# Kernel tuning notes

Measured on AMD Instinct MI355X. Metric: run time of the kernel, lower is better.

## Reference

```python
import jax, jax.numpy as jnp
import numpy as np

EPS = 1e-5
BLOCKS = 8

def _bn(x, g, b, m, v):
    # eval-mode BatchNorm1d over channel dim of [B, C, T]
    return g[:, None] * (x - m[:, None]) * jax.lax.rsqrt(v[:, None] + EPS) + b[:, None]

def _conv1x1(x, w):
    # x: [B, Cin, T], w: [Cout, Cin] -> [B, Cout, T]
    return jnp.einsum('bct,oc->bot', x, w)

def _dwconv(x, w, dil):
    # x: [B, C, T], w: [C, K] depthwise dilated conv, 'same' padding
    C, K = w.shape
    pad = dil * (K - 1) // 2
    return jax.lax.conv_general_dilated(
        x, w[:, None, :], window_strides=(1,), padding=[(pad, pad)],
        rhs_dilation=(dil,), dimension_numbers=('NCH', 'OIH', 'NCH'),
        feature_group_count=C)

def setup_inputs() -> dict:
    key = jax.random.key(0)
    ks = jax.random.split(key, 16)
    B, Cb, H, T, K = 16, 256, 512, 4096, 3
    d = {}
    d['x'] = jax.random.normal(ks[0], (B, Cb, T), jnp.float32)
    d['bn1_gamma'] = jax.random.uniform(ks[1], (BLOCKS, Cb), jnp.float32)
    d['bn1_beta'] = jax.random.normal(ks[2], (BLOCKS, Cb), jnp.float32)
    d['bn1_mean'] = jax.random.normal(ks[3], (BLOCKS, Cb), jnp.float32)
    d['bn1_var'] = jax.random.uniform(ks[4], (BLOCKS, Cb), jnp.float32)
    d['w1'] = jax.random.normal(ks[5], (BLOCKS, H, Cb), jnp.float32)
    d['bn2_gamma'] = jax.random.uniform(ks[6], (BLOCKS, H), jnp.float32)
    d['bn2_beta'] = jax.random.normal(ks[7], (BLOCKS, H), jnp.float32)
    d['bn2_mean'] = jax.random.normal(ks[8], (BLOCKS, H), jnp.float32)
    d['bn2_var'] = jax.random.uniform(ks[9], (BLOCKS, H), jnp.float32)
    d['dw_w'] = jax.random.normal(ks[10], (BLOCKS, H, K), jnp.float32)
    d['bn3_gamma'] = jax.random.uniform(ks[11], (BLOCKS, H), jnp.float32)
    d['bn3_beta'] = jax.random.normal(ks[12], (BLOCKS, H), jnp.float32)
    d['bn3_mean'] = jax.random.normal(ks[13], (BLOCKS, H), jnp.float32)
    d['bn3_var'] = jax.random.uniform(ks[14], (BLOCKS, H), jnp.float32)
    d['w2'] = jax.random.normal(ks[15], (BLOCKS, Cb, H), jnp.float32)
    return d

def reference(x, bn1_gamma, bn1_beta, bn1_mean, bn1_var, w1,
              bn2_gamma, bn2_beta, bn2_mean, bn2_var, dw_w,
              bn3_gamma, bn3_beta, bn3_mean, bn3_var, w2):
    sign = jnp.sign  # binary activation on inputs and weights
    resid = x
    for i in range(BLOCKS):
        dil = 2 ** i
        h = _bn(resid, bn1_gamma[i], bn1_beta[i], bn1_mean[i], bn1_var[i])
        h = _conv1x1(sign(h), sign(w1[i]))                 # 1x1, Cb -> H
        h = _bn(h, bn2_gamma[i], bn2_beta[i], bn2_mean[i], bn2_var[i])
        h = _dwconv(sign(h), sign(dw_w[i]), dil)           # depthwise dilated
        h = _bn(h, bn3_gamma[i], bn3_beta[i], bn3_mean[i], bn3_var[i])
        h = _conv1x1(sign(h), sign(w2[i]))                 # 1x1, H -> Cb
        resid = resid + h
    return resid
```

## Files before the change

kernel.cpp:

```cpp
#include <hip/hip_runtime.h>
#include <stdint.h>

namespace {
constexpr int Bn  = 16;
constexpr int Cc  = 256;
constexpr int Hn  = 512;
constexpr int Tn  = 4096;
constexpr int CWn = Cc / 32;
constexpr int HWn = Hn / 32;
constexpr int TWn = Tn / 32;
constexpr int TC  = 64;
constexpr float EPSf = 1e-5f;
}

typedef __attribute__((ext_vector_type(4)))  int i32x4;
typedef __attribute__((ext_vector_type(16))) int i32x16;

__device__ __forceinline__ uint32_t nib_expand(uint32_t w, int p) {
  return (((w >> p) & 0xFu) * 0x00204081u) & 0x01010101u;
}

__global__ __launch_bounds__(256) void setup_kernel(
    const float* __restrict__ bn1g, const float* __restrict__ bn1b,
    const float* __restrict__ bn1m, const float* __restrict__ bn1v,
    const float* __restrict__ w1,
    const float* __restrict__ bn2g, const float* __restrict__ bn2b,
    const float* __restrict__ bn2m, const float* __restrict__ bn2v,
    const float* __restrict__ dww,
    const float* __restrict__ bn3g, const float* __restrict__ bn3b,
    const float* __restrict__ bn3m, const float* __restrict__ bn3v,
    const float* __restrict__ w2,
    float* __restrict__ thr1, float* __restrict__ thr2, float* __restrict__ thr3,
    uint32_t* __restrict__ dws, uint32_t* __restrict__ W1p,
    uint8_t* __restrict__ W1f, int* __restrict__ Sw1, int* __restrict__ T2i,
    uint8_t* __restrict__ W2uf, int* __restrict__ Sw2)
{
  const int idx = blockIdx.x * 256 + threadIdx.x;
  if (idx < 8 * Hn * CWn) {
    const int w = idx & (CWn - 1);
    const int h = idx >> 3;
    const float* src = w1 + (size_t)h * Cc + w * 32;
    uint32_t word = 0;
#pragma unroll
    for (int j = 0; j < 32; ++j) word |= (uint32_t)(src[j] > 0.f) << j;
    W1p[h * CWn + w] = word;
    atomicAdd(&Sw1[h], (int)__popc(word));
    const int blk = h >> 9, hl = h & 511;
    uint32_t* dst = (uint32_t*)(W1f + (size_t)blk * 131072);
#pragma unroll
    for (int q = 0; q < 8; ++q)
      dst[((w * 2 + (q >> 2)) * 512 + hl) * 4 + (q & 3)] = nib_expand(word, 4 * q);
  } else {
    const int k = idx - 8 * Hn * CWn;
    const int w = k & (HWn - 1);
    const int c = k >> 4;
    const float* src = w2 + (size_t)c * Hn + w * 32;
    uint32_t word = 0;
#pragma unroll
    for (int j = 0; j < 32; ++j) word |= (uint32_t)(src[j] > 0.f) << j;
    atomicAdd(&Sw2[c], (int)__popc(word));
    const int blk = c >> 8, cl = c & 255;
    uint32_t* dst = (uint32_t*)(W2uf + (size_t)blk * 131072);
#pragma unroll
    for (int q = 0; q < 8; ++q)
      dst[((w * 2 + (q >> 2)) * 256 + cl) * 4 + (q & 3)] = nib_expand(word, 4 * q);
  }
  if (idx < 8 * Cc)
    thr1[idx] = bn1m[idx] - bn1b[idx] * sqrtf(bn1v[idx] + EPSf) / bn1g[idx];
  if (idx < 8 * Hn) {
    const float th2 = bn2m[idx] - bn2b[idx] * sqrtf(bn2v[idx] + EPSf) / bn2g[idx];
    thr2[idx] = th2;
    int T;
    if (th2 >= 8.0e6f)       T =  (1 << 24);
    else if (th2 <= -8.0e6f) T = -(1 << 24);
    else if (th2 == th2)     T = (int)floorf(th2) + 1;
    else                     T =  (1 << 24);
    T2i[idx] = T;
    thr3[idx] = bn3m[idx] - bn3b[idx] * sqrtf(bn3v[idx] + EPSf) / bn3g[idx];
    uint32_t dw = 0;
    for (int k2 = 0; k2 < 3; ++k2) dw |= (uint32_t)(dww[(size_t)idx * 3 + k2] > 0.f) << k2;
    dws[idx] = dw;
  }
}

__global__ __launch_bounds__(256) void k1_pack(
    const float* __restrict__ resid, const float* __restrict__ thr1,
    uint32_t* __restrict__ Xp)
{
  const int idx = blockIdx.x * 256 + threadIdx.x;
  const int t  = idx & (Tn - 1);
  const int cw = (idx >> 12) & (CWn - 1);
  const int b  = idx >> 15;
  const float* r = resid + ((size_t)(b * Cc + cw * 32)) * Tn + t;
  uint32_t word = 0;
#pragma unroll
  for (int j = 0; j < 32; ++j)
    word |= (uint32_t)(r[(size_t)j * Tn] > thr1[cw * 32 + j]) << j;
  Xp[((size_t)b * CWn + cw) * Tn + t] = word;
}

__global__ __launch_bounds__(256) void k2_gemm1(
    const uint32_t* __restrict__ Xp, const uint32_t* __restrict__ W1p,
    const float* __restrict__ thr2, uint32_t* __restrict__ Y)
{
  const int bid  = blockIdx.x;
  const int tblk = bid & 15;
  const int og   = (bid >> 4) & 63;
  const int b    = bid >> 10;
  const int t    = tblk * 256 + threadIdx.x;
  const int o    = og * 8;

  const uint32_t* xrow = Xp + (size_t)b * CWn * Tn + t;
  const uint32_t* wrow = W1p + o * CWn;
  int acc[8] = {0, 0, 0, 0, 0, 0, 0, 0};
#pragma unroll
  for (int w = 0; w < CWn; ++w) {
    const uint32_t xw = xrow[(size_t)w * Tn];
#pragma unroll
    for (int r = 0; r < 8; ++r)
      acc[r] += __popc(xw ^ wrow[r * CWn + w]);
  }
  const int lane = threadIdx.x & 63;
#pragma unroll
  for (int r = 0; r < 8; ++r) {
    const float v = (float)(Cc - 2 * acc[r]);
    const uint64_t m = __ballot(v > thr2[o + r]);
    if ((lane & 31) == 0)
      Y[((size_t)b * TWn + (t >> 5)) * Hn + o + r] = (uint32_t)(m >> lane);
  }
}

__global__ __launch_bounds__(512) void k_iter(
    const uint32_t* __restrict__ Yin, const uint32_t* __restrict__ dws,
    const float* __restrict__ thr3,
    const uint8_t* __restrict__ W2uf, const int* __restrict__ Sw2_i,
    const float* __restrict__ rin, float* __restrict__ rout,
    const float* __restrict__ thr1n,
    const uint8_t* __restrict__ W1f_n, const int* __restrict__ Sw1_n,
    const int* __restrict__ T2i_n, uint32_t* __restrict__ Yout,
    int dil, int do_next)
{
  __shared__ __align__(16) uint8_t Zi8[TC * 512];
  __shared__ uint32_t XpL[TC][9];
  __shared__ int   Tc[Hn];
  __shared__ float thr1L[Cc];
  __shared__ int   Sw2x2L[Cc];
  __shared__ int   Sx[TC], Sz[TC];

  const int chunk = blockIdx.x & (Tn / TC - 1);
  const int b     = blockIdx.x >> 6;
  const int tid   = threadIdx.x;
  const int lane  = tid & 63;
  const int wid   = __builtin_amdgcn_readfirstlane(tid >> 6);
  const int lh    = lane & 31;
  const int twL   = lane >> 5;
  const int tw0   = chunk * 2;
  const int half  = lane >> 5;

  if (tid < TC) { Sx[tid] = 0; Sz[tid] = 0; }
  if (tid < Cc) { thr1L[tid] = thr1n[tid]; Sw2x2L[tid] = 2 * Sw2_i[tid]; }
  Tc[tid] = T2i_n[tid] + 2 * Sw1_n[tid] - 256;
  __syncthreads();

  int zcnt = 0;
#pragma unroll
  for (int task = 0; task < 2; ++task) {
    const int hw = wid * 2 + task;
    const int tw = tw0 + twL;
    const int ch = hw * 32 + lh;

    const uint32_t* yb = Yin + (size_t)b * TWn * Hn + ch;
    const uint32_t ycur = yb[(size_t)tw * Hn];
    uint32_t yl, yr, Vl, Vr;
    if (dil >= 32) {
      const int dw = dil >> 5;
      const bool lok = tw >= dw, rok = tw + dw < TWn;
      yl = lok ? yb[(size_t)(tw - dw) * Hn] : 0u;
      yr = rok ? yb[(size_t)(tw + dw) * Hn] : 0u;
      Vl = lok ? ~0u : 0u;
      Vr = rok ? ~0u : 0u;
    } else {
      const uint32_t yp = (tw > 0) ? yb[(size_t)(tw - 1) * Hn] : 0u;
      const uint32_t yn = (tw < TWn - 1) ? yb[(size_t)(tw + 1) * Hn] : 0u;
      yl = (ycur << dil) | ((tw > 0) ? (yp >> (32 - dil)) : 0u);
      yr = (ycur >> dil) | ((tw < TWn - 1) ? (yn << (32 - dil)) : 0u);
      Vl = (tw == 0) ? (~0u << dil) : ~0u;
      Vr = (tw == TWn - 1) ? (~0u >> dil) : ~0u;
    }
    const uint32_t d = dws[ch];
    const uint32_t a  = ((d & 1u) ? yl : ~yl) & Vl;
    const uint32_t bb = (d & 2u) ? ycur : ~ycur;
    const uint32_t c  = ((d & 4u) ? yr : ~yr) & Vr;

    const float thr = thr3[ch];
    const float v3 = (thr + 3.f) * 0.5f;
    const float v2 = (thr + 2.f) * 0.5f;
    const int K3 = (int)(v3 >= 0.f) + (int)(v3 >= 1.f) + (int)(v3 >= 2.f) + (int)(v3 >= 3.f);
    const int K2 = (int)(v2 >= 0.f) + (int)(v2 >= 1.f) + (int)(v2 >= 2.f);

    const uint32_t g1 = a | bb | c;
    const uint32_t g2 = (a & bb) | (c & (a | bb));
    const uint32_t g3 = a & bb & c;
    const uint32_t full = (K3 == 0) ? ~0u : (K3 == 1) ? g1 : (K3 == 2) ? g2
                        : (K3 == 3) ? g3 : 0u;
    const uint32_t lm = (K2 == 0) ? ~0u : (K2 == 1) ? (bb | c) : (K2 == 2) ? (bb & c) : 0u;
    const uint32_t rm = (K2 == 0) ? ~0u : (K2 == 1) ? (a | bb) : (K2 == 2) ? (a & bb) : 0u;

    uint32_t w = (Vl & Vr & full) | (~Vl & lm) | (~Vr & rm);

#pragma unroll
    for (int s = 16; s; s >>= 1) {
      const uint32_t m = 0xFFFFFFFFu / ((1u << s) + 1u);
      const uint32_t o = __shfl_xor(w, s, 64);
      w = ((lane & s) == 0) ? ((w & m) | ((o & m) << s))
                            : ((w & ~m) | ((o & ~m) >> s));
    }
    const int swzA = (lane & 15) << 4;
    uint32_t e[8];
#pragma unroll
    for (int q = 0; q < 8; ++q)
      e[q] = nib_expand(w, 4 * q);
    i32x4 v0; v0[0] = e[0]; v0[1] = e[1]; v0[2] = e[2]; v0[3] = e[3];
    i32x4 v1; v1[0] = e[4]; v1[1] = e[5]; v1[2] = e[6]; v1[3] = e[7];
    *(i32x4*)&Zi8[lane * 512 + ((hw * 32)      ^ swzA)] = v0;
    *(i32x4*)&Zi8[lane * 512 + ((hw * 32 + 16) ^ swzA)] = v1;
    zcnt += (int)__popc(w);
  }
  atomicAdd(&Sz[lane], zcnt);
  __syncthreads();

  {
    const int mc   = wid;
    const int lrow = mc * 32 + lh;
    const int t0   = chunk * TC;

    float rv0[16], rv1[16];
#pragma unroll
    for (int r = 0; r < 16; ++r) {
      const int cr = mc * 32 + (r & 3) + 8 * (r >> 2) + 4 * half;
      const float* rowp = rin + ((size_t)(b * Cc + cr)) * Tn + t0;
      rv0[r] = rowp[lh];
      rv1[r] = rowp[32 + lh];
    }

    const int swz0 = (lh & 15) << 4;
    i32x16 acc0 = {0,0,0,0, 0,0,0,0, 0,0,0,0, 0,0,0,0};
    i32x16 acc1 = {0,0,0,0, 0,0,0,0, 0,0,0,0, 0,0,0,0};
#pragma unroll
    for (int kg = 0; kg < 2; ++kg) {
      i32x4 afv[8];
#pragma unroll
      for (int kk = 0; kk < 8; ++kk) {
        const int ks = kg * 8 + kk;
        afv[kk] = *(const i32x4*)(W2uf + (((size_t)(ks * 2 + half) * 256 + lrow) * 16));
      }
#pragma unroll
      for (int kk = 0; kk < 8; ++kk) {
        const int ks = kg * 8 + kk;
        const int k0 = ks * 32 + half * 16;
        const i32x4 bf0 = *(const i32x4*)&Zi8[lh * 512 + (k0 ^ swz0)];
        const i32x4 bf1 = *(const i32x4*)&Zi8[(32 + lh) * 512 + (k0 ^ swz0)];
        acc0 = __builtin_amdgcn_mfma_i32_32x32x32_i8(afv[kk], bf0, acc0, 0, 0, 0);
        acc1 = __builtin_amdgcn_mfma_i32_32x32x32_i8(afv[kk], bf1, acc1, 0, 0, 0);
      }
    }

    const int Sz0 = 2 * Sz[lh], Sz1 = 2 * Sz[32 + lh];
    uint32_t xw0 = 0, xw1 = 0;
#pragma unroll
    for (int r = 0; r < 16; ++r) {
      const int cloc = (r & 3) + 8 * (r >> 2) + 4 * half;
      const int cr = mc * 32 + cloc;
      const int sw2 = Sw2x2L[cr];
      const float th = thr1L[cr];
      float* orow = rout + ((size_t)(b * Cc + cr)) * Tn + chunk * TC;
      const float ro0 = rv0[r] + (float)((acc0[r] << 2) - Sz0 - sw2 + 512);
      const float ro1 = rv1[r] + (float)((acc1[r] << 2) - Sz1 - sw2 + 512);
      orow[lh]      = ro0;
      orow[32 + lh] = ro1;
      xw0 |= (uint32_t)(ro0 > th) << cloc;
      xw1 |= (uint32_t)(ro1 > th) << cloc;
    }
    const uint32_t ox0 = xw0 | __shfl_xor(xw0, 32, 64);
    const uint32_t ox1 = xw1 | __shfl_xor(xw1, 32, 64);
    if (half == 0) {
      XpL[lh][mc]      = ox0;
      XpL[32 + lh][mc] = ox1;
      atomicAdd(&Sx[lh],      (int)__popc(ox0));
      atomicAdd(&Sx[32 + lh], (int)__popc(ox1));
    }
  }
  __syncthreads();

  if (do_next) {
    const int ntile = wid & 1;
    const int mloc  = wid >> 1;
    const int tloc  = ntile * 32 + lh;
    const int hs    = half * 16;

    i32x4 bf[8];
#pragma unroll
    for (int ks = 0; ks < 8; ++ks) {
      const uint32_t xb = XpL[tloc][ks];
#pragma unroll
      for (int q = 0; q < 4; ++q)
        bf[ks][q] = (int)nib_expand(xb, hs + 4 * q);
    }
    const int Sxv2 = 2 * Sx[tloc];
    uint32_t* yo = Yout + ((size_t)b * TWn + (chunk * 2 + ntile)) * Hn;

#pragma unroll 1
    for (int msup = 0; msup < 4; ++msup) {
      const int row = msup * 128 + mloc * 32 + lh;
      i32x4 afv[8];
#pragma unroll
      for (int ks = 0; ks < 8; ++ks)
        afv[ks] = *(const i32x4*)(W1f_n + (((size_t)(ks * 2 + half) * 512 + row) * 16));
      i32x16 acc = {0,0,0,0, 0,0,0,0, 0,0,0,0, 0,0,0,0};
#pragma unroll
      for (int ks = 0; ks < 8; ++ks)
        acc = __builtin_amdgcn_mfma_i32_32x32x32_i8(afv[ks], bf[ks], acc, 0, 0, 0);

      const int obase = msup * 128 + mloc * 32;
#pragma unroll
      for (int r = 0; r < 16; ++r) {
        const int orow = (r & 3) + 8 * (r >> 2) + 4 * half;
        const int o = obase + orow;
        const uint64_t m = __ballot((acc[r] << 2) >= Tc[o] + Sxv2);
        if ((lane & 31) == 0) yo[o] = (uint32_t)(m >> lane);
      }
    }
  }
}

extern "C" void kernel_launch(void* const* d_in, const int* in_sizes, int n_in,
                              void* d_out, int out_size, void* d_ws, size_t ws_size,
                              hipStream_t stream)
{
  const float* x     = (const float*)d_in[0];
  const float* bn1g  = (const float*)d_in[1];
  const float* bn1b  = (const float*)d_in[2];
  const float* bn1m  = (const float*)d_in[3];
  const float* bn1v  = (const float*)d_in[4];
  const float* w1    = (const float*)d_in[5];
  const float* bn2g  = (const float*)d_in[6];
  const float* bn2b  = (const float*)d_in[7];
  const float* bn2m  = (const float*)d_in[8];
  const float* bn2v  = (const float*)d_in[9];
  const float* dww   = (const float*)d_in[10];
  const float* bn3g  = (const float*)d_in[11];
  const float* bn3b  = (const float*)d_in[12];
  const float* bn3m  = (const float*)d_in[13];
  const float* bn3v  = (const float*)d_in[14];
  const float* w2    = (const float*)d_in[15];
  float* out = (float*)d_out;

  char* ws = (char*)d_ws;
  uint32_t* Xp  = (uint32_t*)(ws);
  uint32_t* Ya  = (uint32_t*)(ws + (2u  << 20));
  uint32_t* Yb  = (uint32_t*)(ws + (6u  << 20));
  uint32_t* W1p = (uint32_t*)(ws + (10u << 20));
  float*    thr1 = (float*)(ws + (10u << 20) + (256u << 10));
  float*    thr2 = thr1 + 8 * Cc;
  float*    thr3 = thr2 + 8 * Hn;
  uint32_t* dws  = (uint32_t*)(thr3 + 8 * Hn);
  uint8_t*  W1f  = (uint8_t*)(ws + (11u << 20));
  int*      Sw1  = (int*)(ws + (12u << 20));
  int*      Sw2  = (int*)(ws + (12u << 20) + (16u << 10));
  int*      T2i  = (int*)(ws + (12u << 20) + (24u << 10));
  uint8_t*  W2uf = (uint8_t*)(ws + (13u << 20));

  hipMemsetAsync(Sw1, 0, (24u << 10), stream);

  setup_kernel<<<256, 256, 0, stream>>>(bn1g, bn1b, bn1m, bn1v, w1,
                                        bn2g, bn2b, bn2m, bn2v, dww,
                                        bn3g, bn3b, bn3m, bn3v, w2,
                                        thr1, thr2, thr3, dws, W1p,
                                        W1f, Sw1, T2i, W2uf, Sw2);

  k1_pack <<<2048,  256, 0, stream>>>(x, thr1, Xp);
  k2_gemm1<<<16384, 256, 0, stream>>>(Xp, W1p, thr2, Ya);

  for (int i = 0; i < 8; ++i) {
    const float* rin = (i == 0) ? x : out;
    const int inext = (i < 7) ? i + 1 : 7;
    const uint32_t* Yin  = (i & 1) ? Yb : Ya;
    uint32_t*       Yout = (i & 1) ? Ya : Yb;
    k_iter<<<1024, 512, 0, stream>>>(Yin, dws + i * Hn, thr3 + i * Hn,
                                     W2uf + (size_t)i * 131072, Sw2 + i * Cc,
                                     rin, out,
                                     thr1 + inext * Cc,
                                     W1f + (size_t)inext * 131072,
                                     Sw1 + inext * Hn, T2i + inext * Hn,
                                     Yout, 1 << i, (i < 7) ? 1 : 0);
  }
}
```

Measured before the change: 405.2 us.

## Halve k_iter time chunk to 32 with 256-thread blocks and swizzled block order

Shrinks the per-block time chunk from 64 to 32 columns and launches twice as many 256-thread blocks. Each wave now covers two channel tiles of the second GEMM in a loop. The next-block activations are stored directly as expanded int8 in a swizzled shared buffer, so the nibble-expansion step before the first GEMM of the next block goes away. Block indices are remapped so adjacent blocks belong to different batches, which may spread memory traffic. The cost is that W2/W1 fragments are reloaded by twice as many blocks, and each block has less MFMA reuse per weight load.

Measured after the change: 586.4 us. 44.7% more time.

```diff
diff --git a/kernel.cpp b/kernel.cpp
--- a/kernel.cpp
+++ b/kernel.cpp
@@ -9,7 +9,7 @@
 constexpr int CWn = Cc / 32;
 constexpr int HWn = Hn / 32;
 constexpr int TWn = Tn / 32;
-constexpr int TC  = 64;
+constexpr int TC  = 32;
 constexpr float EPSf = 1e-5f;
 }
 
@@ -130,7 +130,7 @@
   }
 }
 
-__global__ __launch_bounds__(512) void k_iter(
+__global__ __launch_bounds__(256) void k_iter(
     const uint32_t* __restrict__ Yin, const uint32_t* __restrict__ dws,
     const float* __restrict__ thr3,
     const uint8_t* __restrict__ W2uf, const int* __restrict__ Sw2_i,
@@ -141,32 +141,35 @@
     int dil, int do_next)
 {
   __shared__ __align__(16) uint8_t Zi8[TC * 512];
-  __shared__ uint32_t XpL[TC][9];
+  __shared__ __align__(16) uint8_t Xi8[TC * 256];
   __shared__ int   Tc[Hn];
   __shared__ float thr1L[Cc];
   __shared__ int   Sw2x2L[Cc];
   __shared__ int   Sx[TC], Sz[TC];
 
-  const int chunk = blockIdx.x & (Tn / TC - 1);
-  const int b     = blockIdx.x >> 6;
+  const int bid   = blockIdx.x;
+  const int swzB  = ((bid & 7) << 8) | (bid >> 3);
+  const int chunk = swzB & 127;
+  const int b     = swzB >> 7;
   const int tid   = threadIdx.x;
   const int lane  = tid & 63;
   const int wid   = __builtin_amdgcn_readfirstlane(tid >> 6);
   const int lh    = lane & 31;
   const int twL   = lane >> 5;
-  const int tw0   = chunk * 2;
   const int half  = lane >> 5;
+  const int tw    = chunk;
+  const int t0    = chunk * TC;
 
   if (tid < TC) { Sx[tid] = 0; Sz[tid] = 0; }
-  if (tid < Cc) { thr1L[tid] = thr1n[tid]; Sw2x2L[tid] = 2 * Sw2_i[tid]; }
-  Tc[tid] = T2i_n[tid] + 2 * Sw1_n[tid] - 256;
+  { thr1L[tid] = thr1n[tid]; Sw2x2L[tid] = 2 * Sw2_i[tid]; }
+  Tc[tid]       = T2i_n[tid]       + 2 * Sw1_n[tid]       - 256;
+  Tc[tid + 256] = T2i_n[tid + 256] + 2 * Sw1_n[tid + 256] - 256;
   __syncthreads();
 
   int zcnt = 0;
 #pragma unroll
   for (int task = 0; task < 2; ++task) {
-    const int hw = wid * 2 + task;
-    const int tw = tw0 + twL;
+    const int hw = wid * 4 + task * 2 + twL;
     const int ch = hw * 32 + lh;
 
     const uint32_t* yb = Yin + (size_t)b * TWn * Hn + ch;
@@ -215,102 +218,88 @@
       w = ((lane & s) == 0) ? ((w & m) | ((o & m) << s))
                             : ((w & ~m) | ((o & ~m) >> s));
     }
-    const int swzA = (lane & 15) << 4;
+    const int swzA = (lh & 15) << 4;
     uint32_t e[8];
 #pragma unroll
     for (int q = 0; q < 8; ++q)
       e[q] = nib_expand(w, 4 * q);
     i32x4 v0; v0[0] = e[0]; v0[1] = e[1]; v0[2] = e[2]; v0[3] = e[3];
     i32x4 v1; v1[0] = e[4]; v1[1] = e[5]; v1[2] = e[6]; v1[3] = e[7];
-    *(i32x4*)&Zi8[lane * 512 + ((hw * 32)      ^ swzA)] = v0;
-    *(i32x4*)&Zi8[lane * 512 + ((hw * 32 + 16) ^ swzA)] = v1;
+    *(i32x4*)&Zi8[lh * 512 + ((hw * 32)      ^ swzA)] = v0;
+    *(i32x4*)&Zi8[lh * 512 + ((hw * 32 + 16) ^ swzA)] = v1;
     zcnt += (int)__popc(w);
   }
-  atomicAdd(&Sz[lane], zcnt);
+  atomicAdd(&Sz[lh], zcnt);
   __syncthreads();
 
   {
-    const int mc   = wid;
-    const int lrow = mc * 32 + lh;
-    const int t0   = chunk * TC;
-
-    float rv0[16], rv1[16];
-#pragma unroll
-    for (int r = 0; r < 16; ++r) {
-      const int cr = mc * 32 + (r & 3) + 8 * (r >> 2) + 4 * half;
-      const float* rowp = rin + ((size_t)(b * Cc + cr)) * Tn + t0;
-      rv0[r] = rowp[lh];
-      rv1[r] = rowp[32 + lh];
-    }
-
     const int swz0 = (lh & 15) << 4;
-    i32x16 acc0 = {0,0,0,0, 0,0,0,0, 0,0,0,0, 0,0,0,0};
-    i32x16 acc1 = {0,0,0,0, 0,0,0,0, 0,0,0,0, 0,0,0,0};
-#pragma unroll
-    for (int kg = 0; kg < 2; ++kg) {
-      i32x4 afv[8];
-#pragma unroll
-      for (int kk = 0; kk < 8; ++kk) {
-        const int ks = kg * 8 + kk;
-        afv[kk] = *(const i32x4*)(W2uf + (((size_t)(ks * 2 + half) * 256 + lrow) * 16));
-      }
-#pragma unroll
-      for (int kk = 0; kk < 8; ++kk) {
-        const int ks = kg * 8 + kk;
-        const int k0 = ks * 32 + half * 16;
-        const i32x4 bf0 = *(const i32x4*)&Zi8[lh * 512 + (k0 ^ swz0)];
-        const i32x4 bf1 = *(const i32x4*)&Zi8[(32 + lh) * 512 + (k0 ^ swz0)];
-        acc0 = __builtin_amdgcn_mfma_i32_32x32x32_i8(afv[kk], bf0, acc0, 0, 0, 0);
-        acc1 = __builtin_amdgcn_mfma_i32_32x32x32_i8(afv[kk], bf1, acc1, 0, 0, 0);
-      }
-    }
-
-    const int Sz0 = 2 * Sz[lh], Sz1 = 2 * Sz[32 + lh];
-    uint32_t xw0 = 0, xw1 = 0;
-#pragma unroll
-    for (int r = 0; r < 16; ++r) {
-      const int cloc = (r & 3) + 8 * (r >> 2) + 4 * half;
-      const int cr = mc * 32 + cloc;
-      const int sw2 = Sw2x2L[cr];
-      const float th = thr1L[cr];
-      float* orow = rout + ((size_t)(b * Cc + cr)) * Tn + chunk * TC;
-      const float ro0 = rv0[r] + (float)((acc0[r] << 2) - Sz0 - sw2 + 512);
-      const float ro1 = rv1[r] + (float)((acc1[r] << 2) - Sz1 - sw2 + 512);
-      orow[lh]      = ro0;
-      orow[32 + lh] = ro1;
-      xw0 |= (uint32_t)(ro0 > th) << cloc;
-      xw1 |= (uint32_t)(ro1 > th) << cloc;
-    }
-    const uint32_t ox0 = xw0 | __shfl_xor(xw0, 32, 64);
-    const uint32_t ox1 = xw1 | __shfl_xor(xw1, 32, 64);
-    if (half == 0) {
-      XpL[lh][mc]      = ox0;
-      XpL[32 + lh][mc] = ox1;
-      atomicAdd(&Sx[lh],      (int)__popc(ox0));
-      atomicAdd(&Sx[32 + lh], (int)__popc(ox1));
+    const int Szv2 = 2 * Sz[lh];
+#pragma unroll 1
+    for (int ct = 0; ct < 2; ++ct) {
+      const int mc   = wid + ct * 4;
+      const int lrow = mc * 32 + lh;
+
+      float rv[16];
+#pragma unroll
+      for (int r = 0; r < 16; ++r) {
+        const int cr = mc * 32 + (r & 3) + 8 * (r >> 2) + 4 * half;
+        rv[r] = rin[((size_t)(b * Cc + cr)) * Tn + t0 + lh];
+      }
+
+      i32x16 acc = {0,0,0,0, 0,0,0,0, 0,0,0,0, 0,0,0,0};
+#pragma unroll
+      for (int kg = 0; kg < 2; ++kg) {
+        i32x4 afv[8];
+#pragma unroll
+        for (int kk = 0; kk < 8; ++kk) {
+          const int ks = kg * 8 + kk;
+          afv[kk] = *(const i32x4*)(W2uf + (((size_t)(ks * 2 + half) * 256 + lrow) * 16));
+        }
+#pragma unroll
+        for (int kk = 0; kk < 8; ++kk) {
+          const int ks = kg * 8 + kk;
+          const int k0 = ks * 32 + half * 16;
+          const i32x4 bf = *(const i32x4*)&Zi8[lh * 512 + (k0 ^ swz0)];
+          acc = __builtin_amdgcn_mfma_i32_32x32x32_i8(afv[kk], bf, acc, 0, 0, 0);
+        }
+      }
+
+      uint32_t dw[4] = {0, 0, 0, 0};
+#pragma unroll
+      for (int r = 0; r < 16; ++r) {
+        const int cloc = (r & 3) + 8 * (r >> 2) + 4 * half;
+        const int cr = mc * 32 + cloc;
+        const float ro = rv[r] + (float)((acc[r] << 2) - Szv2 - Sw2x2L[cr] + 512);
+        rout[((size_t)(b * Cc + cr)) * Tn + t0 + lh] = ro;
+        dw[r >> 2] |= (uint32_t)(ro > thr1L[cr]) << ((r & 3) * 8);
+      }
+      int cnt = 0;
+#pragma unroll
+      for (int g = 0; g < 4; ++g) {
+        const int cb = mc * 32 + g * 8 + half * 4;
+        *(uint32_t*)&Xi8[lh * 256 + (cb ^ swz0)] = dw[g];
+        cnt += __popc(dw[g]);
+      }
+      atomicAdd(&Sx[lh], cnt);
     }
   }
   __syncthreads();
 
   if (do_next) {
-    const int ntile = wid & 1;
-    const int mloc  = wid >> 1;
-    const int tloc  = ntile * 32 + lh;
-    const int hs    = half * 16;
-
+    const int tloc = lh;
     i32x4 bf[8];
 #pragma unroll
     for (int ks = 0; ks < 8; ++ks) {
-      const uint32_t xb = XpL[tloc][ks];
-#pragma unroll
-      for (int q = 0; q < 4; ++q)
-        bf[ks][q] = (int)nib_expand(xb, hs + 4 * q);
+      const int koff = (ks * 32 + half * 16) ^ ((tloc & 15) << 4);
+      bf[ks] = *(const i32x4*)&Xi8[tloc * 256 + koff];
     }
     const int Sxv2 = 2 * Sx[tloc];
-    uint32_t* yo = Yout + ((size_t)b * TWn + (chunk * 2 + ntile)) * Hn;
+    uint32_t* yo = Yout + ((size_t)b * TWn + chunk) * Hn;
+    const int msup = wid;
 
 #pragma unroll 1
-    for (int msup = 0; msup < 4; ++msup) {
+    for (int mloc = 0; mloc < 4; ++mloc) {
       const int row = msup * 128 + mloc * 32 + lh;
       i32x4 afv[8];
 #pragma unroll
@@ -386,7 +375,7 @@
     const int inext = (i < 7) ? i + 1 : 7;
     const uint32_t* Yin  = (i & 1) ? Yb : Ya;
     uint32_t*       Yout = (i & 1) ? Ya : Yb;
-    k_iter<<<1024, 512, 0, stream>>>(Yin, dws + i * Hn, thr3 + i * Hn,
+    k_iter<<<2048, 256, 0, stream>>>(Yin, dws + i * Hn, thr3 + i * Hn,
                                      W2uf + (size_t)i * 131072, Sw2 + i * Cc,
                                      rin, out,
                                      thr1 + inext * Cc,
```
